# Kernel optimization log

Hardware: AMD Instinct MI355X
Metric: run time of the kernel (lower is better)

Reference implementation:

```python
import jax, jax.numpy as jnp
import numpy as np
import math

B, S, D, H = 4, 2048, 1024, 16
DK = D // H

def setup_inputs() -> dict:
    key = jax.random.key(0)
    ks = jax.random.split(key, 6)
    scale = 1.0 / math.sqrt(D)
    x = jax.random.normal(ks[0], (B, S, D), dtype=jnp.float32)
    mask = jnp.tril(jnp.ones((S, S), dtype=jnp.int32))[None, None]  # [1,1,S,S] causal
    Wq = jax.random.normal(ks[1], (D, D), dtype=jnp.float32) * scale
    Wk = jax.random.normal(ks[2], (D, D), dtype=jnp.float32) * scale
    Wv = jax.random.normal(ks[3], (D, D), dtype=jnp.float32) * scale
    Wo = jax.random.normal(ks[4], (D, D), dtype=jnp.float32) * scale
    z = jnp.zeros((D,), dtype=jnp.float32)
    return {"x": x, "mask": mask, "Wq": Wq, "bq": z, "Wk": Wk, "bk": z,
            "Wv": Wv, "bv": z, "Wo": Wo, "bo": z}

def reference(x, mask, Wq, bq, Wk, bk, Wv, bv, Wo, bo):
    bsz, seq_len, d_model = x.shape
    def split_heads(t):  # [B,S,D] -> [B,H,S,DK]
        return t.reshape(bsz, seq_len, H, DK).transpose(0, 2, 1, 3)
    Q = split_heads(x @ Wq + bq)
    K = split_heads(x @ Wk + bk)
    V = split_heads(x @ Wv + bv)
    scores = jnp.einsum('bhqd,bhkd->bhqk', Q, K) / jnp.sqrt(jnp.asarray(DK, x.dtype))
    scores = jnp.where(mask == 0, jnp.asarray(-jnp.inf, x.dtype), scores)
    attn = jax.nn.softmax(scores, axis=-1)
    # dropout is identity in eval mode
    context = jnp.einsum('bhqk,bhkd->bhqd', attn, V)
    context = context.transpose(0, 2, 1, 3).reshape(bsz, seq_len, d_model)
    return context @ Wo + bo
```

## Files before the change

kernel.cpp:

```cpp
#include <hip/hip_runtime.h>
#include <hip/hip_bf16.h>
#include <math.h>

#define BATCH 4
#define SEQ   2048
#define DMODEL 1024
#define NHEAD 16
#define DHEAD 64
#define MROWS (BATCH * SEQ)
#define SC_Q  0.1803368801111244f

typedef __attribute__((ext_vector_type(8))) short short8;
typedef __attribute__((ext_vector_type(4))) short short4_t;
typedef __attribute__((ext_vector_type(4))) float f32x4;
typedef __attribute__((ext_vector_type(4))) unsigned short ushort4v;

__device__ inline unsigned short f2bf(float f) {
    union { float f; unsigned int u; } v; v.f = f;
    unsigned int r = v.u + 0x7FFFu + ((v.u >> 16) & 1u);
    return (unsigned short)(r >> 16);
}

__device__ inline unsigned int cvt_pk_bf16(float a, float b) {
    unsigned int r;
    asm("v_cvt_pk_bf16_f32 %0, %1, %2" : "=v"(r) : "v"(a), "v"(b));
    return r;
}

__device__ __forceinline__ void g2l16(const unsigned short* g, unsigned short* l) {
    __builtin_amdgcn_global_load_lds(
        (const __attribute__((address_space(1))) unsigned int*)g,
        (__attribute__((address_space(3))) unsigned int*)l, 16, 0, 0);
}

__global__ __launch_bounds__(256) void cvt_bf16_kernel(
    const float* __restrict__ src, unsigned short* __restrict__ dst, int n4)
{
    const int i = blockIdx.x * 256 + threadIdx.x;
    if (i < n4) {
        float4 v = ((const float4*)src)[i];
        ushort4v o = { f2bf(v.x), f2bf(v.y), f2bf(v.z), f2bf(v.w) };
        ((ushort4v*)dst)[i] = o;
    }
}

__global__ __launch_bounds__(256) void bias_pack_kernel(
    const float* __restrict__ bq, const float* __restrict__ bk,
    const float* __restrict__ bv, float* __restrict__ b3)
{
    const int i = blockIdx.x * 256 + threadIdx.x;
    if (i < DMODEL) {
        b3[i]              = bq[i];
        b3[i + DMODEL]     = bk[i];
        b3[i + 2 * DMODEL] = bv[i];
    }
}

__global__ __launch_bounds__(256) void transpose_cvt_kernel(
    const float* __restrict__ W0, const float* __restrict__ W1,
    const float* __restrict__ W2, const float* __restrict__ W3,
    unsigned short* __restrict__ T0, unsigned short* __restrict__ T1,
    unsigned short* __restrict__ T2, unsigned short* __restrict__ T3)
{
    const float* W; unsigned short* T;
    switch (blockIdx.z) {
        case 0: W = W0; T = T0; break;
        case 1: W = W1; T = T1; break;
        case 2: W = W2; T = T2; break;
        default: W = W3; T = T3; break;
    }
    __shared__ float tile[32][33];
    const int r0 = blockIdx.y * 32, c0 = blockIdx.x * 32;
    const int c = threadIdx.x & 31, r = threadIdx.x >> 5;
    #pragma unroll
    for (int i = 0; i < 4; ++i)
        tile[r + i * 8][c] = W[(size_t)(r0 + r + i * 8) * DMODEL + c0 + c];
    __syncthreads();
    #pragma unroll
    for (int i = 0; i < 4; ++i)
        T[(size_t)(c0 + r + i * 8) * DMODEL + r0 + c] = f2bf(tile[c][r + i * 8]);
}

__global__ __launch_bounds__(256) void transpose_v_kernel(
    const unsigned short* __restrict__ Vin, unsigned short* __restrict__ Vt)
{
    __shared__ unsigned short t[64][72];
    const int tid = threadIdx.x;
    const int kt = blockIdx.x, bh = blockIdx.y;
    const unsigned short* src = Vin + ((size_t)bh * SEQ + kt * 64) * DHEAD;
    const int r = tid >> 3, c = (tid & 7) * 8;
    *(short8*)&t[r][c]      = *(const short8*)(src + (size_t)r * DHEAD + c);
    *(short8*)&t[r + 32][c] = *(const short8*)(src + (size_t)(r + 32) * DHEAD + c);
    __syncthreads();
    unsigned short* dst = Vt + (size_t)bh * DHEAD * SEQ + kt * 64;
    const int d = tid >> 3, k0 = (tid & 7) * 8;
    short8 v0, v1;
    #pragma unroll
    for (int i = 0; i < 8; ++i) {
        v0[i] = (short)t[k0 + i][d];
        v1[i] = (short)t[k0 + i][d + 32];
    }
    *(short8*)(dst + (size_t)d * SEQ + k0)        = v0;
    *(short8*)(dst + (size_t)(d + 32) * SEQ + k0) = v1;
}

__global__ __launch_bounds__(256) void gemm_qkv(
    const unsigned short* __restrict__ A, const unsigned short* __restrict__ Bt,
    const float* __restrict__ bias3, unsigned short* __restrict__ QKV )
{
    __shared__ unsigned short As[128 * 32];
    __shared__ unsigned short Bs[128 * 32];

    const int tid  = threadIdx.x;
    const int wave = tid >> 6, lane = tid & 63;
    const int l15  = lane & 15, quad = lane >> 4;
    const int wm   = (wave >> 1) * 64;
    const int wn   = (wave & 1) * 64;
    const int m0   = blockIdx.y * 128;
    const int n0   = blockIdx.x * 128;
    const int Kdim = DMODEL;

    f32x4 acc[4][4];
    #pragma unroll
    for (int i = 0; i < 4; ++i)
        #pragma unroll
        for (int j = 0; j < 4; ++j) acc[i][j] = (f32x4){0.f, 0.f, 0.f, 0.f};

    const int c_lo = wave * 64 + lane;

    for (int k0 = 0; k0 < Kdim; k0 += 32) {
        __syncthreads();
        {
            int c = c_lo;
            g2l16(A  + (size_t)(m0 + (c >> 2)) * Kdim + k0 + (c & 3) * 8, As + c * 8);
            g2l16(Bt + (size_t)(n0 + (c >> 2)) * Kdim + k0 + (c & 3) * 8, Bs + c * 8);
            c = c_lo + 256;
            g2l16(A  + (size_t)(m0 + (c >> 2)) * Kdim + k0 + (c & 3) * 8, As + c * 8);
            g2l16(Bt + (size_t)(n0 + (c >> 2)) * Kdim + k0 + (c & 3) * 8, Bs + c * 8);
        }
        __syncthreads();

        short8 af[4], bf[4];
        #pragma unroll
        for (int mi = 0; mi < 4; ++mi)
            af[mi] = *(const short8*)&As[(wm + mi * 16 + l15) * 32 + quad * 8];
        #pragma unroll
        for (int ni = 0; ni < 4; ++ni)
            bf[ni] = *(const short8*)&Bs[(wn + ni * 16 + l15) * 32 + quad * 8];
        #pragma unroll
        for (int mi = 0; mi < 4; ++mi)
            #pragma unroll
            for (int ni = 0; ni < 4; ++ni)
                acc[mi][ni] = __builtin_amdgcn_mfma_f32_16x16x32_bf16(
                    af[mi], bf[ni], acc[mi][ni], 0, 0, 0);
    }

    const size_t elems = (size_t)MROWS * DMODEL;
    #pragma unroll
    for (int mi = 0; mi < 4; ++mi) {
        #pragma unroll
        for (int r = 0; r < 4; ++r) {
            const int m = m0 + wm + mi * 16 + quad * 4 + r;
            const int b = m >> 11, s = m & 2047;
            #pragma unroll
            for (int ni = 0; ni < 4; ++ni) {
                const int n   = n0 + wn + ni * 16 + l15;
                const int seg = n >> 10, nn = n & 1023;
                const int h = nn >> 6, dk = nn & 63;
                const float sc  = (seg == 0) ? SC_Q : 1.0f;
                const float val = (acc[mi][ni][r] + bias3[n]) * sc;
                QKV[seg * elems + (((size_t)(b * NHEAD + h)) * SEQ + s) * DHEAD + dk] = f2bf(val);
            }
        }
    }
}

__global__ __launch_bounds__(256) void gemm_out(
    const unsigned short* __restrict__ A, const unsigned short* __restrict__ Bt,
    const float* __restrict__ bias, float* __restrict__ Cout)
{
    __shared__ unsigned short As[128 * 32];
    __shared__ unsigned short Bs[128 * 32];

    const int tid  = threadIdx.x;
    const int wave = tid >> 6, lane = tid & 63;
    const int l15  = lane & 15, quad = lane >> 4;
    const int wm   = (wave >> 1) * 64;
    const int wn   = (wave & 1) * 64;
    const int m0   = blockIdx.y * 128;
    const int n0   = blockIdx.x * 128;
    const int Kdim = DMODEL, Ndim = DMODEL;

    f32x4 acc[4][4];
    #pragma unroll
    for (int i = 0; i < 4; ++i)
        #pragma unroll
        for (int j = 0; j < 4; ++j) acc[i][j] = (f32x4){0.f, 0.f, 0.f, 0.f};

    const int c_lo = wave * 64 + lane;

    for (int k0 = 0; k0 < Kdim; k0 += 32) {
        __syncthreads();
        {
            int c = c_lo;
            g2l16(A  + (size_t)(m0 + (c >> 2)) * Kdim + k0 + (c & 3) * 8, As + c * 8);
            g2l16(Bt + (size_t)(n0 + (c >> 2)) * Kdim + k0 + (c & 3) * 8, Bs + c * 8);
            c = c_lo + 256;
            g2l16(A  + (size_t)(m0 + (c >> 2)) * Kdim + k0 + (c & 3) * 8, As + c * 8);
            g2l16(Bt + (size_t)(n0 + (c >> 2)) * Kdim + k0 + (c & 3) * 8, Bs + c * 8);
        }
        __syncthreads();

        short8 af[4], bf[4];
        #pragma unroll
        for (int mi = 0; mi < 4; ++mi)
            af[mi] = *(const short8*)&As[(wm + mi * 16 + l15) * 32 + quad * 8];
        #pragma unroll
        for (int ni = 0; ni < 4; ++ni)
            bf[ni] = *(const short8*)&Bs[(wn + ni * 16 + l15) * 32 + quad * 8];
        #pragma unroll
        for (int mi = 0; mi < 4; ++mi)
            #pragma unroll
            for (int ni = 0; ni < 4; ++ni)
                acc[mi][ni] = __builtin_amdgcn_mfma_f32_16x16x32_bf16(
                    af[mi], bf[ni], acc[mi][ni], 0, 0, 0);
    }

    #pragma unroll
    for (int mi = 0; mi < 4; ++mi) {
        #pragma unroll
        for (int r = 0; r < 4; ++r) {
            const int m = m0 + wm + mi * 16 + quad * 4 + r;
            #pragma unroll
            for (int ni = 0; ni < 4; ++ni) {
                const int n = n0 + wn + ni * 16 + l15;
                Cout[(size_t)m * Ndim + n] = acc[mi][ni][r] + bias[n];
            }
        }
    }
}

__global__ __launch_bounds__(256, 4) void attn_mfma6(
    const unsigned short* __restrict__ Q, const unsigned short* __restrict__ K,
    const unsigned short* __restrict__ VtG, unsigned short* __restrict__ ctx_out)
{
    __shared__ alignas(16) unsigned short Ks[64 * 64];
    __shared__ alignas(16) unsigned short Vts[64 * 64];

    const int tid  = threadIdx.x;
    const int wave = tid >> 6, lane = tid & 63;
    const int l15  = lane & 15, quad = lane >> 4;
    const int qa   = blockIdx.x;
    const int qb   = 31 - qa;
    const int bh   = blockIdx.y;
    const int b    = bh >> 4, h = bh & 15;

    const unsigned short* Kb0 = K   + (size_t)bh * SEQ * DHEAD;
    const unsigned short* Vb0 = VtG + (size_t)bh * DHEAD * SEQ;

    short8 qf[2][2];
    #pragma unroll
    for (int g = 0; g < 2; ++g) {
        const int qtile = g ? qb : qa;
        const unsigned short* qrow =
            Q + ((size_t)bh * SEQ + qtile * 64 + wave * 16 + l15) * DHEAD + quad * 8;
        qf[g][0] = *(const short8*)qrow;
        qf[g][1] = *(const short8*)(qrow + 32);
    }

    f32x4 Of[2][4];
    float lsum[2] = {0.f, 0.f};
    #pragma unroll
    for (int g = 0; g < 2; ++g)
        #pragma unroll
        for (int i = 0; i < 4; ++i) Of[g][i] = (f32x4){0.f, 0.f, 0.f, 0.f};

    const int qloc = wave * 16 + l15;
    const f32x4 zero4 = (f32x4){0.f, 0.f, 0.f, 0.f};

    short8 kreg[2], vreg[2];
    #pragma unroll
    for (int i = 0; i < 2; ++i) {
        const int c = tid + i * 256;
        const int kk = c >> 3, qs = c & 7;
        const int gq = qs ^ (kk & 7);
        kreg[i] = *(const short8*)(Kb0 + (size_t)kk * DHEAD + gq * 8);
        vreg[i] = *(const short8*)(Vb0 + (size_t)kk * SEQ   + gq * 8);
    }

    for (int jb = 0; jb <= qb; ++jb) {
        __syncthreads();
        #pragma unroll
        for (int i = 0; i < 2; ++i) {
            const int c = tid + i * 256;
            *(short8*)&Ks[c * 8]  = kreg[i];
            *(short8*)&Vts[c * 8] = vreg[i];
        }
        __syncthreads();

        const bool act0  = (jb <= qa);
        const bool diag0 = (jb == qa);
        const bool diag1 = (jb == qb);

        short4_t pw[2][4];
        #pragma unroll
        for (int nt = 0; nt < 4; ++nt) {
            const int k = nt * 16 + l15;
            const short8 a0 = *(const short8*)&Ks[(k * 8 + ( quad      ^ (k & 7))) * 8];
            const short8 a1 = *(const short8*)&Ks[(k * 8 + ((quad + 4) ^ (k & 7))) * 8];

            f32x4 s1 = __builtin_amdgcn_mfma_f32_16x16x32_bf16(a0, qf[1][0], zero4, 0, 0, 0);
            s1       = __builtin_amdgcn_mfma_f32_16x16x32_bf16(a1, qf[1][1], s1,    0, 0, 0);
            f32x4 p1;
            #pragma unroll
            for (int r = 0; r < 4; ++r) p1[r] = __builtin_amdgcn_exp2f(s1[r]);
            if (diag1) {
                #pragma unroll
                for (int r = 0; r < 4; ++r)
                    if (nt * 16 + quad * 4 + r > qloc) p1[r] = 0.f;
            }
            lsum[1] += (p1[0] + p1[1]) + (p1[2] + p1[3]);
            union { unsigned int u[2]; short4_t v; } pk1;
            pk1.u[0] = cvt_pk_bf16(p1[0], p1[1]);
            pk1.u[1] = cvt_pk_bf16(p1[2], p1[3]);
            pw[1][nt] = pk1.v;

            if (act0) {
                f32x4 s0 = __builtin_amdgcn_mfma_f32_16x16x32_bf16(a0, qf[0][0], zero4, 0, 0, 0);
                s0       = __builtin_amdgcn_mfma_f32_16x16x32_bf16(a1, qf[0][1], s0,    0, 0, 0);
                f32x4 p0;
                #pragma unroll
                for (int r = 0; r < 4; ++r) p0[r] = __builtin_amdgcn_exp2f(s0[r]);
                if (diag0) {
                    #pragma unroll
                    for (int r = 0; r < 4; ++r)
                        if (nt * 16 + quad * 4 + r > qloc) p0[r] = 0.f;
                }
                lsum[0] += (p0[0] + p0[1]) + (p0[2] + p0[3]);
                union { unsigned int u[2]; short4_t v; } pk0;
                pk0.u[0] = cvt_pk_bf16(p0[0], p0[1]);
                pk0.u[1] = cvt_pk_bf16(p0[2], p0[3]);
                pw[0][nt] = pk0.v;
            }
        }

        if (jb < qb) {
            const unsigned short* Kt  = Kb0 + (size_t)(jb + 1) * 64 * DHEAD;
            const unsigned short* Vt0 = Vb0 + (jb + 1) * 64;
            #pragma unroll
            for (int i = 0; i < 2; ++i) {
                const int c = tid + i * 256;
                const int kk = c >> 3, qs = c & 7;
                const int gq = qs ^ (kk & 7);
                kreg[i] = *(const short8*)(Kt  + (size_t)kk * DHEAD + gq * 8);
                vreg[i] = *(const short8*)(Vt0 + (size_t)kk * SEQ   + gq * 8);
            }
        }

        #pragma unroll
        for (int kc = 0; kc < 4; ++kc) {
            #pragma unroll
            for (int nt = 0; nt < 4; ++nt) {
                const int d  = nt * 16 + l15;
                const int kb = kc * 2 + (quad >> 1);
                const short4_t vb = *(const short4_t*)
                    &Vts[(d * 8 + (kb ^ (d & 7))) * 8 + (quad & 1) * 4];
                Of[1][nt] = __builtin_amdgcn_mfma_f32_16x16x16bf16_1k(
                    pw[1][kc], vb, Of[1][nt], 0, 0, 0);
                if (act0)
                    Of[0][nt] = __builtin_amdgcn_mfma_f32_16x16x16bf16_1k(
                        pw[0][kc], vb, Of[0][nt], 0, 0, 0);
            }
        }
    }

    #pragma unroll
    for (int g = 0; g < 2; ++g) {
        const int qtile = g ? qb : qa;
        float l = lsum[g];
        l += __shfl_xor(l, 16);
        l += __shfl_xor(l, 32);
        #pragma unroll
        for (int r = 0; r < 4; ++r) {
            const float inv = 1.0f / __shfl(l, quad * 4 + r);
            const int s = qtile * 64 + wave * 16 + quad * 4 + r;
            unsigned short* o = ctx_out + ((size_t)(b * SEQ + s)) * DMODEL + h * DHEAD;
            #pragma unroll
            for (int nt = 0; nt < 4; ++nt)
                o[nt * 16 + l15] = f2bf(Of[g][nt][r] * inv);
        }
    }
}

extern "C" void kernel_launch(void* const* d_in, const int* in_sizes, int n_in,
                              void* d_out, int out_size, void* d_ws, size_t ws_size,
                              hipStream_t stream) {
    const float* x  = (const float*)d_in[0];
    const float* Wq = (const float*)d_in[2];
    const float* bq = (const float*)d_in[3];
    const float* Wk = (const float*)d_in[4];
    const float* bk = (const float*)d_in[5];
    const float* Wv = (const float*)d_in[6];
    const float* bv = (const float*)d_in[7];
    const float* Wo = (const float*)d_in[8];
    const float* bo = (const float*)d_in[9];
    float* out = (float*)d_out;

    const size_t elems  = (size_t)MROWS * DMODEL;
    const size_t welems = (size_t)DMODEL * DMODEL;
    unsigned short* xbf   = (unsigned short*)d_ws;
    unsigned short* WqkvT = xbf + elems;
    unsigned short* WoT   = WqkvT + 3 * welems;
    unsigned short* Qbuf  = WoT + welems;
    unsigned short* Kbuf  = Qbuf + elems;
    unsigned short* Vbuf  = Kbuf + elems;
    unsigned short* VtG   = Vbuf + elems;
    unsigned short* Cbuf  = VtG + elems;
    float*          bias3 = (float*)(Cbuf + elems);

    dim3 blk(256);

    cvt_bf16_kernel<<<dim3((int)(elems / 4 / 256)), blk, 0, stream>>>(x, xbf, (int)(elems / 4));
    transpose_cvt_kernel<<<dim3(32, 32, 4), blk, 0, stream>>>(
        Wq, Wk, Wv, Wo, WqkvT, WqkvT + welems, WqkvT + 2 * welems, WoT);
    bias_pack_kernel<<<dim3(4), blk, 0, stream>>>(bq, bk, bv, bias3);

    dim3 gqkv(3 * DMODEL / 128, MROWS / 128);
    gemm_qkv<<<gqkv, blk, 0, stream>>>(xbf, WqkvT, bias3, Qbuf);

    transpose_v_kernel<<<dim3(SEQ / 64, BATCH * NHEAD), blk, 0, stream>>>(Vbuf, VtG);

    dim3 gattn(16, BATCH * NHEAD);
    attn_mfma6<<<gattn, blk, 0, stream>>>(Qbuf, Kbuf, VtG, Cbuf);

    dim3 gout(DMODEL / 128, MROWS / 128);
    gemm_out<<<gout, blk, 0, stream>>>(Cbuf, WoT, bo, out);
}
```

Baseline: 325.0 us.

## Double-buffer K/V via async global-to-LDS loads and use K=32 MFMA for PV

The attention kernel now stages K and V tiles directly into double-buffered LDS with global_load_lds, which removes the register round-trip and one barrier per iteration. The next tile's load overlaps compute on the current one. The V transpose kernel permutes the key order within each 64-tile so the PV product can use 16x16x32 bf16 MFMAs with packed 8-element P fragments, halving the PV MFMA count. LDS use doubles, which may limit occupancy, and the s_waitcnt vmcnt(0) still serialises each stage.

Measured after the change: 289.7 us. 1.12x faster.

```diff
diff --git a/kernel.cpp b/kernel.cpp
--- a/kernel.cpp
+++ b/kernel.cpp
@@ -11,7 +11,6 @@
 #define SC_Q  0.1803368801111244f
 
 typedef __attribute__((ext_vector_type(8))) short short8;
-typedef __attribute__((ext_vector_type(4))) short short4_t;
 typedef __attribute__((ext_vector_type(4))) float f32x4;
 typedef __attribute__((ext_vector_type(4))) unsigned short ushort4v;
 
@@ -93,15 +92,17 @@
     *(short8*)&t[r + 32][c] = *(const short8*)(src + (size_t)(r + 32) * DHEAD + c);
     __syncthreads();
     unsigned short* dst = Vt + (size_t)bh * DHEAD * SEQ + kt * 64;
-    const int d = tid >> 3, k0 = (tid & 7) * 8;
+    const int d = tid >> 3, p0 = (tid & 7) * 8;
     short8 v0, v1;
     #pragma unroll
     for (int i = 0; i < 8; ++i) {
-        v0[i] = (short)t[k0 + i][d];
-        v1[i] = (short)t[k0 + i][d + 32];
-    }
-    *(short8*)(dst + (size_t)d * SEQ + k0)        = v0;
-    *(short8*)(dst + (size_t)(d + 32) * SEQ + k0) = v1;
+        const int p = p0 + i;
+        const int k = (p & 32) | (((p >> 2) & 1) << 4) | (((p >> 3) & 3) << 2) | (p & 3);
+        v0[i] = (short)t[k][d];
+        v1[i] = (short)t[k][d + 32];
+    }
+    *(short8*)(dst + (size_t)d * SEQ + p0)        = v0;
+    *(short8*)(dst + (size_t)(d + 32) * SEQ + p0) = v1;
 }
 
 __global__ __launch_bounds__(256) void gemm_qkv(
@@ -240,12 +241,12 @@
     }
 }
 
-__global__ __launch_bounds__(256, 4) void attn_mfma6(
+__global__ __launch_bounds__(256, 4) void attn_mfma7(
     const unsigned short* __restrict__ Q, const unsigned short* __restrict__ K,
     const unsigned short* __restrict__ VtG, unsigned short* __restrict__ ctx_out)
 {
-    __shared__ alignas(16) unsigned short Ks[64 * 64];
-    __shared__ alignas(16) unsigned short Vts[64 * 64];
+    __shared__ alignas(16) unsigned short Ks[2][64 * 64];
+    __shared__ alignas(16) unsigned short Vs[2][64 * 64];
 
     const int tid  = threadIdx.x;
     const int wave = tid >> 6, lane = tid & 63;
@@ -278,36 +279,43 @@
     const int qloc = wave * 16 + l15;
     const f32x4 zero4 = (f32x4){0.f, 0.f, 0.f, 0.f};
 
-    short8 kreg[2], vreg[2];
-    #pragma unroll
-    for (int i = 0; i < 2; ++i) {
-        const int c = tid + i * 256;
-        const int kk = c >> 3, qs = c & 7;
-        const int gq = qs ^ (kk & 7);
-        kreg[i] = *(const short8*)(Kb0 + (size_t)kk * DHEAD + gq * 8);
-        vreg[i] = *(const short8*)(Vb0 + (size_t)kk * SEQ   + gq * 8);
-    }
+    const int ck0 = tid >> 3, cg0 = tid & 7;
+    const int ck1 = (tid + 256) >> 3, cg1 = tid & 7;
+
+    #define STAGE(buf, jb)                                                          \
+        do {                                                                        \
+            const unsigned short* Kt_ = Kb0 + (size_t)(jb) * 64 * DHEAD;            \
+            const unsigned short* Vt_ = Vb0 + (jb) * 64;                            \
+            g2l16(Kt_ + (size_t)ck0 * DHEAD + (cg0 ^ (ck0 & 7)) * 8,                \
+                  &Ks[buf][(tid) * 8]);                                             \
+            g2l16(Vt_ + (size_t)ck0 * SEQ   + (cg0 ^ (ck0 & 7)) * 8,                \
+                  &Vs[buf][(tid) * 8]);                                             \
+            g2l16(Kt_ + (size_t)ck1 * DHEAD + (cg1 ^ (ck1 & 7)) * 8,                \
+                  &Ks[buf][(tid + 256) * 8]);                                       \
+            g2l16(Vt_ + (size_t)ck1 * SEQ   + (cg1 ^ (ck1 & 7)) * 8,                \
+                  &Vs[buf][(tid + 256) * 8]);                                       \
+        } while (0)
+
+    STAGE(0, 0);
 
     for (int jb = 0; jb <= qb; ++jb) {
+        const int cur = jb & 1;
+        asm volatile("s_waitcnt vmcnt(0)" ::: "memory");
         __syncthreads();
-        #pragma unroll
-        for (int i = 0; i < 2; ++i) {
-            const int c = tid + i * 256;
-            *(short8*)&Ks[c * 8]  = kreg[i];
-            *(short8*)&Vts[c * 8] = vreg[i];
-        }
-        __syncthreads();
+        if (jb < qb) STAGE(cur ^ 1, jb + 1);
 
         const bool act0  = (jb <= qa);
         const bool diag0 = (jb == qa);
         const bool diag1 = (jb == qb);
-
-        short4_t pw[2][4];
+        const unsigned short* KsC = &Ks[cur][0];
+        const unsigned short* VsC = &Vs[cur][0];
+
+        union { unsigned int u[4]; short8 v; } pa[2][2];
         #pragma unroll
         for (int nt = 0; nt < 4; ++nt) {
             const int k = nt * 16 + l15;
-            const short8 a0 = *(const short8*)&Ks[(k * 8 + ( quad      ^ (k & 7))) * 8];
-            const short8 a1 = *(const short8*)&Ks[(k * 8 + ((quad + 4) ^ (k & 7))) * 8];
+            const short8 a0 = *(const short8*)&KsC[(k * 8 + ( quad      ^ (k & 7))) * 8];
+            const short8 a1 = *(const short8*)&KsC[(k * 8 + ((quad + 4) ^ (k & 7))) * 8];
 
             f32x4 s1 = __builtin_amdgcn_mfma_f32_16x16x32_bf16(a0, qf[1][0], zero4, 0, 0, 0);
             s1       = __builtin_amdgcn_mfma_f32_16x16x32_bf16(a1, qf[1][1], s1,    0, 0, 0);
@@ -320,10 +328,8 @@
                     if (nt * 16 + quad * 4 + r > qloc) p1[r] = 0.f;
             }
             lsum[1] += (p1[0] + p1[1]) + (p1[2] + p1[3]);
-            union { unsigned int u[2]; short4_t v; } pk1;
-            pk1.u[0] = cvt_pk_bf16(p1[0], p1[1]);
-            pk1.u[1] = cvt_pk_bf16(p1[2], p1[3]);
-            pw[1][nt] = pk1.v;
+            pa[1][nt >> 1].u[(nt & 1) * 2]     = cvt_pk_bf16(p1[0], p1[1]);
+            pa[1][nt >> 1].u[(nt & 1) * 2 + 1] = cvt_pk_bf16(p1[2], p1[3]);
 
             if (act0) {
                 f32x4 s0 = __builtin_amdgcn_mfma_f32_16x16x32_bf16(a0, qf[0][0], zero4, 0, 0, 0);
@@ -337,42 +343,27 @@
                         if (nt * 16 + quad * 4 + r > qloc) p0[r] = 0.f;
                 }
                 lsum[0] += (p0[0] + p0[1]) + (p0[2] + p0[3]);
-                union { unsigned int u[2]; short4_t v; } pk0;
-                pk0.u[0] = cvt_pk_bf16(p0[0], p0[1]);
-                pk0.u[1] = cvt_pk_bf16(p0[2], p0[3]);
-                pw[0][nt] = pk0.v;
+                pa[0][nt >> 1].u[(nt & 1) * 2]     = cvt_pk_bf16(p0[0], p0[1]);
+                pa[0][nt >> 1].u[(nt & 1) * 2 + 1] = cvt_pk_bf16(p0[2], p0[3]);
             }
         }
 
-        if (jb < qb) {
-            const unsigned short* Kt  = Kb0 + (size_t)(jb + 1) * 64 * DHEAD;
-            const unsigned short* Vt0 = Vb0 + (jb + 1) * 64;
-            #pragma unroll
-            for (int i = 0; i < 2; ++i) {
-                const int c = tid + i * 256;
-                const int kk = c >> 3, qs = c & 7;
-                const int gq = qs ^ (kk & 7);
-                kreg[i] = *(const short8*)(Kt  + (size_t)kk * DHEAD + gq * 8);
-                vreg[i] = *(const short8*)(Vt0 + (size_t)kk * SEQ   + gq * 8);
+        #pragma unroll
+        for (int cc = 0; cc < 2; ++cc) {
+            #pragma unroll
+            for (int nt = 0; nt < 4; ++nt) {
+                const int d = nt * 16 + l15;
+                const short8 vb = *(const short8*)
+                    &VsC[(d * 8 + ((cc * 4 + quad) ^ (d & 7))) * 8];
+                Of[1][nt] = __builtin_amdgcn_mfma_f32_16x16x32_bf16(
+                    pa[1][cc].v, vb, Of[1][nt], 0, 0, 0);
+                if (act0)
+                    Of[0][nt] = __builtin_amdgcn_mfma_f32_16x16x32_bf16(
+                        pa[0][cc].v, vb, Of[0][nt], 0, 0, 0);
             }
         }
-
-        #pragma unroll
-        for (int kc = 0; kc < 4; ++kc) {
-            #pragma unroll
-            for (int nt = 0; nt < 4; ++nt) {
-                const int d  = nt * 16 + l15;
-                const int kb = kc * 2 + (quad >> 1);
-                const short4_t vb = *(const short4_t*)
-                    &Vts[(d * 8 + (kb ^ (d & 7))) * 8 + (quad & 1) * 4];
-                Of[1][nt] = __builtin_amdgcn_mfma_f32_16x16x16bf16_1k(
-                    pw[1][kc], vb, Of[1][nt], 0, 0, 0);
-                if (act0)
-                    Of[0][nt] = __builtin_amdgcn_mfma_f32_16x16x16bf16_1k(
-                        pw[0][kc], vb, Of[0][nt], 0, 0, 0);
-            }
-        }
-    }
+    }
+    #undef STAGE
 
     #pragma unroll
     for (int g = 0; g < 2; ++g) {
@@ -431,7 +422,7 @@
     transpose_v_kernel<<<dim3(SEQ / 64, BATCH * NHEAD), blk, 0, stream>>>(Vbuf, VtG);
 
     dim3 gattn(16, BATCH * NHEAD);
-    attn_mfma6<<<gattn, blk, 0, stream>>>(Qbuf, Kbuf, VtG, Cbuf);
+    attn_mfma7<<<gattn, blk, 0, stream>>>(Qbuf, Kbuf, VtG, Cbuf);
 
     dim3 gout(DMODEL / 128, MROWS / 128);
     gemm_out<<<gout, blk, 0, stream>>>(Cbuf, WoT, bo, out);
```
